# Kernel optimization log

Hardware: AMD Instinct MI355X
Metric: run time of the kernel (lower is better)

Reference implementation:

```python
import jax, jax.numpy as jnp
import numpy as np
import math

DIM = 512
NUM_HEADS = 8
DIM_HEAD = DIM // NUM_HEADS


def normalized_coords(h, w):
    # (h*w, 2) with (x, y) in [0, 1]
    y = jnp.linspace(0.0, 1.0, h)
    x = jnp.linspace(0.0, 1.0, w)
    yg, xg = jnp.meshgrid(y, x, indexing='ij')
    return jnp.stack([xg.ravel(), yg.ravel()], axis=-1)


def rotate_half(x):
    dh = x.shape[-1] // 2
    return jnp.concatenate([-x[..., dh:], x[..., :dh]], axis=-1)


def apply_rope(t, coords):
    # t: (n, heads, seq, dim_head); coords: (seq, 2) (identical across batch)
    dim_half = t.shape[-1] // 2
    freq = 1.0 / (10000.0 ** (jnp.arange(dim_half, dtype=jnp.float32) / dim_half))
    ang_x = coords[:, 0:1] * freq  # (seq, dim_half)
    ang_y = coords[:, 1:2] * freq
    ang = jnp.concatenate([ang_x, ang_y], axis=-1)  # (seq, dim_head)
    cos, sin = jnp.cos(ang), jnp.sin(ang)
    return t * cos + rotate_half(t) * sin


def setup_inputs() -> dict:
    key = jax.random.key(0)
    ks = jax.random.split(key, 12)
    n, Np, d, H, W = 4, 1024, DIM, 64, 64
    s = 0.02
    return {
        'local_feat': jax.random.normal(ks[0], (n, Np, d), jnp.float32),
        'global_feat': jax.random.normal(ks[1], (n, d, H, W), jnp.float32),
        'Wq': jax.random.normal(ks[2], (d, d), jnp.float32) * s,
        'bq': jnp.zeros((d,), jnp.float32),
        'Wk': jax.random.normal(ks[3], (d, d), jnp.float32) * s,
        'bk': jnp.zeros((d,), jnp.float32),
        'Wv': jax.random.normal(ks[4], (d, d), jnp.float32) * s,
        'bv': jnp.zeros((d,), jnp.float32),
        'Wg': jax.random.normal(ks[5], (d, 2 * d), jnp.float32) * s,
        'bg': jnp.zeros((d,), jnp.float32),
        'Wo': jax.random.normal(ks[6], (d, d), jnp.float32) * s,
        'bo': jnp.zeros((d,), jnp.float32),
    }


def reference(local_feat, global_feat, Wq, bq, Wk, bk, Wv, bv, Wg, bg, Wo, bo):
    n, Np, d = local_feat.shape
    _, _, H, W = global_feat.shape
    h, dh = NUM_HEADS, DIM_HEAD
    gf = global_feat.reshape(n, d, H * W).transpose(0, 2, 1)  # (n, HW, d)

    P = int(math.isqrt(Np))
    local_coords = normalized_coords(P, P)      # (Np, 2)
    global_coords = normalized_coords(H, W)     # (HW, 2)

    def proj(x, Wt, b):
        return x @ Wt.T + b

    Q = proj(local_feat, Wq, bq).reshape(n, Np, h, dh).transpose(0, 2, 1, 3)
    K = proj(gf, Wk, bk).reshape(n, H * W, h, dh).transpose(0, 2, 1, 3)
    V = proj(gf, Wv, bv).reshape(n, H * W, h, dh).transpose(0, 2, 1, 3)

    Q = apply_rope(Q, local_coords)
    K = apply_rope(K, global_coords)

    scores = jnp.einsum('bhqd,bhkd->bhqk', Q, K) / math.sqrt(dh)
    attn = jax.nn.softmax(scores, axis=-1)
    ao = jnp.einsum('bhqk,bhkd->bhqd', attn, V)
    ao = ao.transpose(0, 2, 1, 3).reshape(n, Np, d)

    gate = jax.nn.sigmoid(jnp.concatenate([local_feat, ao], axis=-1) @ Wg.T + bg)
    enhanced = local_feat + gate * ao
    return enhanced @ Wo.T + bo
```

## Files before the change

### kernel.cpp

```cpp
#include <hip/hip_runtime.h>
#include <hip/hip_bf16.h>
#include <cstdint>

typedef __hip_bfloat16 BF;
typedef unsigned short ushort_t;
typedef __attribute__((ext_vector_type(8))) __bf16 bf16x8;
typedef __attribute__((ext_vector_type(4))) float f32x4;
typedef __attribute__((ext_vector_type(4))) unsigned uint4v;

__device__ __forceinline__ float bu2f(ushort_t u) {
  return __uint_as_float((unsigned)u << 16);
}
__device__ __forceinline__ unsigned pk2(float a, float b) {
  union { __hip_bfloat162 h; unsigned u; } c;
  c.h = __float22bfloat162_rn(make_float2(a, b));
  return c.u;
}
__device__ __forceinline__ unsigned short f2bu(float f) {
  union { BF b; unsigned short u; } c; c.b = __float2bfloat16(f); return c.u;
}
__device__ __forceinline__ float b2f(BF x) { return __bfloat162float(x); }
__device__ __forceinline__ void rd16f(const float* fp, ushort_t* out) {
#pragma unroll
  for (int j = 0; j < 16; j += 4) {
    float4 v = *(const float4*)(fp + j);
    ((unsigned*)out)[j / 2] = pk2(v.x, v.y);
    ((unsigned*)out)[j / 2 + 1] = pk2(v.z, v.w);
  }
}

#define QS 0.1803368801111f

__global__ __launch_bounds__(256) void prep_k(const float* __restrict__ local,
                                              const float* __restrict__ Wq,
                                              const float* __restrict__ Wk,
                                              const float* __restrict__ Wv,
                                              const float* __restrict__ Wg,
                                              const float* __restrict__ Wo,
                                              BF* __restrict__ localB,
                                              BF* __restrict__ WB) {
  size_t e = ((size_t)blockIdx.x * 256 + threadIdx.x) * 16;
  const float* src;
  BF* dst;
  if (e < 2097152) {
    src = local + e;  dst = localB + e;
  } else {
    size_t f = e - 2097152;
    dst = WB + f;
    if (f < 262144)        src = Wq + f;
    else if (f < 524288)   src = Wk + (f - 262144);
    else if (f < 786432)   src = Wv + (f - 524288);
    else if (f < 1310720)  src = Wg + (f - 786432);
    else                   src = Wo + (f - 1310720);
  }
  ushort_t vals[16];
  rd16f(src, vals);
  *(uint4*)dst = *(uint4*)&vals[0];
  *((uint4*)dst + 1) = *(uint4*)&vals[8];
}

__global__ __launch_bounds__(256) void pre_k(const float* __restrict__ local,
                                             const float* __restrict__ gfeat,
                                             const float* __restrict__ Wq,
                                             const float* __restrict__ bq,
                                             const BF* __restrict__ localB,
                                             const BF* __restrict__ WqB,
                                             BF* __restrict__ gfT,
                                             BF* __restrict__ Qb) {
  __shared__ __align__(16) ushort_t smem[2][64][72];
  const int t = threadIdx.x;
  if (blockIdx.x < 2048) {
    auto T = smem[0];
    const int g = blockIdx.x;
    const int bz = g & 3, mt = (g >> 2) & 63, kt = g >> 8;
    {
      int krow = t >> 2, mg = t & 3;
      ushort_t vals[16];
      rd16f(gfeat + (size_t)bz * 512 * 4096 + (size_t)(kt * 64 + krow) * 4096 +
                mt * 64 + mg * 16,
            vals);
#pragma unroll
      for (int j = 0; j < 16; ++j) T[mg * 16 + j][krow] = vals[j];
    }
    __syncthreads();
    int mrow = t >> 2, kg = t & 3;
    uint4 a = *(const uint4*)&T[mrow][kg * 16];
    uint4 b = *(const uint4*)&T[mrow][kg * 16 + 8];
    size_t o = ((size_t)bz * 4096 + mt * 64 + mrow) * 512 + kt * 64 + kg * 16;
    *(uint4*)&gfT[o] = a;
    *(uint4*)&gfT[o + 8] = b;
    return;
  }
  auto As = smem[0];
  auto Bs = smem[1];
  const int bx = blockIdx.x - 2048;
  const int m0 = (bx & 63) * 64, n0 = (bx >> 6) * 64;
  const int w = t >> 6, lane = t & 63;
  const int quad = lane >> 4, l16 = lane & 15;

  f32x4 acc[4] = {};
  for (int k0 = 0; k0 < 512; k0 += 64) {
    __syncthreads();
    {
      int row = t >> 2, cg = t & 3;
      int kg = k0 + cg * 16;
      if (WqB) {
        const uint4* pa = (const uint4*)(localB + (size_t)(m0 + row) * 512 + kg);
        *(uint4*)&As[row][cg * 16] = pa[0];
        *(uint4*)&As[row][cg * 16 + 8] = pa[1];
        const uint4* pb = (const uint4*)(WqB + (size_t)(n0 + row) * 512 + kg);
        *(uint4*)&Bs[row][cg * 16] = pb[0];
        *(uint4*)&Bs[row][cg * 16 + 8] = pb[1];
      } else {
        ushort_t vals[16];
        rd16f(local + (size_t)(m0 + row) * 512 + kg, vals);
        *(uint4*)&As[row][cg * 16] = *(uint4*)&vals[0];
        *(uint4*)&As[row][cg * 16 + 8] = *(uint4*)&vals[8];
        ushort_t bv[16];
        rd16f(Wq + (size_t)(n0 + row) * 512 + kg, bv);
        *(uint4*)&Bs[row][cg * 16] = *(uint4*)&bv[0];
        *(uint4*)&Bs[row][cg * 16 + 8] = *(uint4*)&bv[8];
      }
    }
    __syncthreads();
#pragma unroll
    for (int kc = 0; kc < 2; ++kc) {
      bf16x8 af = *(const bf16x8*)&As[w * 16 + l16][kc * 32 + quad * 8];
#pragma unroll
      for (int nt = 0; nt < 4; ++nt) {
        bf16x8 bfv = *(const bf16x8*)&Bs[nt * 16 + l16][kc * 32 + quad * 8];
        acc[nt] = __builtin_amdgcn_mfma_f32_16x16x32_bf16(af, bfv, acc[nt], 0, 0, 0);
      }
    }
  }
  const int head = n0 >> 6;
#pragma unroll
  for (int r = 0; r < 4; ++r) {
    int mg = m0 + w * 16 + quad * 4 + r;
    int bb = mg >> 10, qi = mg & 1023;
    float x = (float)(qi & 31) * (1.f / 31.f);
    float y = (float)(qi >> 5) * (1.f / 31.f);
    size_t base = (((size_t)bb * 8 + head) * 1024 + qi) * 64;
#pragma unroll
    for (int j = 0; j < 2; ++j) {
      int c0 = j * 16 + l16;
      float t0 = acc[j][r] + bq[head * 64 + c0];
      float t1 = acc[j + 2][r] + bq[head * 64 + c0 + 32];
      float fr = __expf((float)c0 * (-9.210340371976184f / 32.f));
      float ax = x * fr, ay = y * fr;
      Qb[base + c0] = __float2bfloat16((t0 * __cosf(ax) - t1 * __sinf(ax)) * QS);
      Qb[base + c0 + 32] = __float2bfloat16((t1 * __cosf(ay) + t0 * __sinf(ay)) * QS);
    }
  }
}

__global__ __launch_bounds__(256) void kv_k(const BF* __restrict__ gfT,
                                            const float* __restrict__ Wk,
                                            const float* __restrict__ Wv,
                                            const BF* __restrict__ WkB,
                                            const BF* __restrict__ WvB,
                                            const float* __restrict__ bk,
                                            const float* __restrict__ bv,
                                            BF* __restrict__ Kb,
                                            BF* __restrict__ VTb) {
  __shared__ __align__(16) ushort_t smem[2][128][72];
  auto As = smem[0];
  auto Bs = smem[1];
  const int tid = threadIdx.x;
  const int w = tid >> 6, lane = tid & 63;
  const int quad = lane >> 4, l16 = lane & 15;
  const int wm = w >> 1, wn = w & 1;
  const int g = blockIdx.x;
  const int a = g & 7, y = (g >> 3) & 7, bidx = g >> 6;
  const int m0 = ((bidx << 1) | (a & 1)) * 128;
  const int n0 = y * 128;
  const int bz = a >> 1;

  f32x4 acc[4][4] = {};
  for (int k0 = 0; k0 < 512; k0 += 64) {
    __syncthreads();
#pragma unroll
    for (int u = 0; u < 2; ++u) {
      int unit = tid + u * 256;
      int row = unit >> 2, cg = unit & 3;
      const uint4* p = (const uint4*)(gfT + ((size_t)bz * 4096 + m0 + row) * 512 +
                                      k0 + cg * 16);
      *(uint4*)&As[row][cg * 16] = p[0];
      *(uint4*)&As[row][cg * 16 + 8] = p[1];
    }
    if (WkB) {
      const BF* bb16 = (n0 >= 512) ? WvB : WkB;
      const int nb = (n0 >= 512) ? (n0 - 512) : n0;
#pragma unroll
      for (int u = 0; u < 2; ++u) {
        int unit = tid + u * 256;
        int row = unit >> 2, cg = unit & 3;
        const uint4* p = (const uint4*)(bb16 + (size_t)(nb + row) * 512 +
                                        k0 + cg * 16);
        *(uint4*)&Bs[row][cg * 16] = p[0];
        *(uint4*)&Bs[row][cg * 16 + 8] = p[1];
      }
    } else {
#pragma unroll
      for (int u = 0; u < 2; ++u) {
        int unit = tid + u * 256;
        int row = unit >> 2, cg = unit & 3;
        const float* bsrc = (n0 >= 512) ? Wv : Wk;
        size_t nrow = (n0 >= 512) ? (n0 - 512 + row) : (n0 + row);
        ushort_t vals[16];
        rd16f(bsrc + nrow * 512 + k0 + cg * 16, vals);
        *(uint4*)&Bs[row][cg * 16] = *(uint4*)&vals[0];
        *(uint4*)&Bs[row][cg * 16 + 8] = *(uint4*)&vals[8];
      }
    }
    __syncthreads();
#pragma unroll
    for (int kc = 0; kc < 2; ++kc) {
      bf16x8 af[4], bfv[4];
#pragma unroll
      for (int i = 0; i < 4; ++i) {
        af[i] = *(const bf16x8*)&As[wm * 64 + i * 16 + l16][kc * 32 + quad * 8];
        bfv[i] = *(const bf16x8*)&Bs[wn * 64 + i * 16 + l16][kc * 32 + quad * 8];
      }
#pragma unroll
      for (int mt = 0; mt < 4; ++mt)
#pragma unroll
        for (int nt = 0; nt < 4; ++nt)
          acc[mt][nt] = __builtin_amdgcn_mfma_f32_16x16x32_bf16(af[mt], bfv[nt], acc[mt][nt], 0, 0, 0);
    }
  }
  if (n0 < 512) {
    const int head = (n0 + wn * 64) >> 6;
#pragma unroll
    for (int mt = 0; mt < 4; ++mt)
#pragma unroll
      for (int r = 0; r < 4; ++r) {
        int pg = m0 + wm * 64 + mt * 16 + quad * 4 + r;
        float x = (float)(pg & 63) * (1.f / 63.f);
        float yy = (float)(pg >> 6) * (1.f / 63.f);
        size_t base = (((size_t)bz * 8 + head) * 4096 + pg) * 64;
#pragma unroll
        for (int j = 0; j < 2; ++j) {
          int c0 = j * 16 + l16;
          float t0 = acc[mt][j][r] + bk[head * 64 + c0];
          float t1 = acc[mt][j + 2][r] + bk[head * 64 + c0 + 32];
          float fr = __expf((float)c0 * (-9.210340371976184f / 32.f));
          float ax = x * fr, ay = yy * fr;
          Kb[base + c0] = __float2bfloat16(t0 * __cosf(ax) - t1 * __sinf(ax));
          Kb[base + c0 + 32] = __float2bfloat16(t1 * __cosf(ay) + t0 * __sinf(ay));
        }
      }
  } else {
    const int n0v = n0 - 512;
    __syncthreads();
    ushort_t (*T)[136] = (ushort_t(*)[136]) & smem[0][0][0];
#pragma unroll
    for (int mt = 0; mt < 4; ++mt)
#pragma unroll
      for (int nt = 0; nt < 4; ++nt)
#pragma unroll
        for (int r = 0; r < 4; ++r) {
          int n_l = wn * 64 + nt * 16 + l16;
          int m_l = wm * 64 + mt * 16 + quad * 4 + r;
          T[n_l][m_l] = f2bu(acc[mt][nt][r] + bv[n0v + n_l]);
        }
    __syncthreads();
    int row = tid >> 1, half = tid & 1;
    size_t gbase = (((size_t)bz * 8 + (n0v >> 6) + (row >> 6)) * 64 + (row & 63)) * 4096 +
                   m0 + half * 64;
    uint4* dst = (uint4*)(VTb + gbase);
    const uint4* src = (const uint4*)&T[row][half * 64];
#pragma unroll
    for (int j = 0; j < 8; ++j) dst[j] = src[j];
  }
}

template <int NS>
__global__ __launch_bounds__(256, 4) void attn_k(const BF* __restrict__ Q,
                                                 const BF* __restrict__ K,
                                                 const BF* __restrict__ VT,
                                                 BF* __restrict__ AO,
                                                 BF* __restrict__ Opart,
                                                 float* __restrict__ lpart) {
  __shared__ __align__(16) ushort_t Ks[2][64][64];
  __shared__ __align__(16) ushort_t VTs[3][64][64];

  const int tid = threadIdx.x;
  const int w = tid >> 6, lane = tid & 63;
  const int quad = lane >> 4, l16 = lane & 15;
  const int r3 = l16 & 7;
  const int sc0 = (quad ^ r3) << 3;
  const int sc1 = sc0 ^ 32;

  const int g = blockIdx.x;
  const int bh = g & 31;
  const int qt = (g >> 5) & 7;
  const int ks = g >> 8;
  const int b = bh >> 3, h = bh & 7;
  const int q0 = qt * 128 + w * 32;
  const int kspan = 4096 / NS, kbase = ks * kspan;

  bf16x8 qa[2][2];
#pragma unroll
  for (int qs = 0; qs < 2; ++qs) {
    const BF* qp = Q + (((size_t)bh << 10) + q0 + qs * 16 + l16) * 64 + quad * 8;
    qa[qs][0] = *(const bf16x8*)qp;
    qa[qs][1] = *(const bf16x8*)(qp + 32);
  }
  bf16x8 ones;
#pragma unroll
  for (int j = 0; j < 8; ++j) ones[j] = (__bf16)1.0f;

  const BF* Kp = K + (size_t)bh * 4096 * 64;
  const BF* VTp = VT + (size_t)bh * 64 * 4096;

  f32x4 o[2][4] = {};
  f32x4 ol[2] = {};

  const int srow = tid >> 2, scol = (tid & 3) * 16;
  const int ssc = ((2 * (tid & 3)) ^ (srow & 7)) << 3;
  int vcol[4];
  {
    const int s1 = (tid >> 1) & 1, s0v = tid & 1;
#pragma unroll
    for (int gq = 0; gq < 4; ++gq)
      vcol[gq] = (((s1 * 4 + gq) ^ (srow & 7)) << 3) + s0v * 4;
  }

#define STAGE_V(buf, v0, v1)                                   \
  {                                                            \
    uint2 t_;                                                  \
    t_.x = (v0).x; t_.y = (v0).y; *(uint2*)&VTs[buf][srow][vcol[0]] = t_; \
    t_.x = (v0).z; t_.y = (v0).w; *(uint2*)&VTs[buf][srow][vcol[1]] = t_; \
    t_.x = (v1).x; t_.y = (v1).y; *(uint2*)&VTs[buf][srow][vcol[2]] = t_; \
    t_.x = (v1).z; t_.y = (v1).w; *(uint2*)&VTs[buf][srow][vcol[3]] = t_; \
  }

  {
    const uint4* kp = (const uint4*)(Kp + (size_t)(kbase + srow) * 64 + scol);
    const uint4* vp = (const uint4*)(VTp + (size_t)srow * 4096 + kbase + scol);
    uint4 a = kp[0], bb = kp[1], c = vp[0], d = vp[1];
    *(uint4*)&Ks[0][srow][ssc] = a;  *(uint4*)&Ks[0][srow][ssc ^ 8] = bb;
    STAGE_V(0, c, d);
  }
  __syncthreads();

  bf16x8 pa[2][2];

#define S_PHASE(KRD)                                                          \
  {                                                                           \
    unsigned pu[2][2][4];                                                     \
    _Pragma("unroll") for (int ct = 0; ct < 4; ++ct) {                        \
      const int krow = ct * 16 + l16;                                         \
      bf16x8 kb0 = *(const bf16x8*)&Ks[KRD][krow][sc0];                       \
      bf16x8 kb1 = *(const bf16x8*)&Ks[KRD][krow][sc1];                       \
      _Pragma("unroll") for (int qs = 0; qs < 2; ++qs) {                      \
        f32x4 s = {};                                                         \
        s = __builtin_amdgcn_mfma_f32_16x16x32_bf16(kb0, qa[qs][0], s, 0, 0, 0); \
        s = __builtin_amdgcn_mfma_f32_16x16x32_bf16(kb1, qa[qs][1], s, 0, 0, 0); \
        pu[qs][ct >> 1][(ct & 1) * 2] =                                       \
            pk2(__builtin_exp2f(s[0]), __builtin_exp2f(s[1]));                \
        pu[qs][ct >> 1][(ct & 1) * 2 + 1] =                                   \
            pk2(__builtin_exp2f(s[2]), __builtin_exp2f(s[3]));                \
      }                                                                       \
    }                                                                         \
    _Pragma("unroll") for (int qs = 0; qs < 2; ++qs)                          \
      _Pragma("unroll") for (int kk = 0; kk < 2; ++kk) {                      \
        uint4v u = {pu[qs][kk][0], pu[qs][kk][1], pu[qs][kk][2],              \
                    pu[qs][kk][3]};                                           \
        pa[qs][kk] = __builtin_bit_cast(bf16x8, u);                           \
      }                                                                       \
  }

#define PV_PHASE(VRD)                                                         \
  {                                                                           \
    _Pragma("unroll") for (int qs = 0; qs < 2; ++qs) {                        \
      ol[qs] = __builtin_amdgcn_mfma_f32_16x16x32_bf16(ones, pa[qs][0], ol[qs], 0, 0, 0); \
      ol[qs] = __builtin_amdgcn_mfma_f32_16x16x32_bf16(ones, pa[qs][1], ol[qs], 0, 0, 0); \
    }                                                                         \
    _Pragma("unroll") for (int nt = 0; nt < 4; ++nt) {                        \
      const int vrow = nt * 16 + l16;                                         \
      bf16x8 vb0 = *(const bf16x8*)&VTs[VRD][vrow][sc0];                      \
      bf16x8 vb1 = *(const bf16x8*)&VTs[VRD][vrow][sc1];                      \
      _Pragma("unroll") for (int qs = 0; qs < 2; ++qs) {                      \
        o[qs][nt] = __builtin_amdgcn_mfma_f32_16x16x32_bf16(vb0, pa[qs][0], o[qs][nt], 0, 0, 0); \
        o[qs][nt] = __builtin_amdgcn_mfma_f32_16x16x32_bf16(vb1, pa[qs][1], o[qs][nt], 0, 0, 0); \
      }                                                                       \
    }                                                                         \
  }

  const int nc = kspan / 64;
  {
    uint4 nk0, nk1, nv0, nv1;
    const bool more = (nc > 1);
    if (more) {
      const int c1 = kbase + 64;
      const uint4* kp = (const uint4*)(Kp + (size_t)(c1 + srow) * 64 + scol);
      const uint4* vp = (const uint4*)(VTp + (size_t)srow * 4096 + c1 + scol);
      nk0 = kp[0]; nk1 = kp[1]; nv0 = vp[0]; nv1 = vp[1];
    }
    __builtin_amdgcn_s_setprio(1);
    S_PHASE(0);
    __builtin_amdgcn_s_setprio(0);
    if (more) {
      *(uint4*)&Ks[1][srow][ssc] = nk0;
      *(uint4*)&Ks[1][srow][ssc ^ 8] = nk1;
      STAGE_V(1, nv0, nv1);
    }
    __syncthreads();
  }

  int krd = 1, vrd = 0, vwr = 2;
  for (int c = 1; c < nc; ++c) {
    uint4 nk0, nk1, nv0, nv1;
    const bool more = (c + 1 < nc);
    if (more) {
      const int c1 = kbase + (c + 1) * 64;
      const uint4* kp = (const uint4*)(Kp + (size_t)(c1 + srow) * 64 + scol);
      const uint4* vp = (const uint4*)(VTp + (size_t)srow * 4096 + c1 + scol);
      nk0 = kp[0]; nk1 = kp[1]; nv0 = vp[0]; nv1 = vp[1];
    }
    __builtin_amdgcn_s_setprio(1);
    PV_PHASE(vrd);
    S_PHASE(krd);
    __builtin_amdgcn_s_setprio(0);
    if (more) {
      *(uint4*)&Ks[krd ^ 1][srow][ssc] = nk0;
      *(uint4*)&Ks[krd ^ 1][srow][ssc ^ 8] = nk1;
      STAGE_V(vwr, nv0, nv1);
    }
    __syncthreads();
    krd ^= 1;
    vrd = (vrd == 2) ? 0 : vrd + 1;
    vwr = (vwr == 2) ? 0 : vwr + 1;
  }
  PV_PHASE(vrd);
#undef STAGE_V
#undef S_PHASE
#undef PV_PHASE

#pragma unroll
  for (int qs = 0; qs < 2; ++qs) {
    int qg = q0 + qs * 16 + l16;
    if (NS == 1) {
      float invl = 1.f / ol[qs][0];
#pragma unroll
      for (int nt = 0; nt < 4; ++nt) {
        uint2 uu;
        uu.x = pk2(o[qs][nt][0] * invl, o[qs][nt][1] * invl);
        uu.y = pk2(o[qs][nt][2] * invl, o[qs][nt][3] * invl);
        *(uint2*)(AO + (((size_t)b << 10) + qg) * 512 + h * 64 + nt * 16 + quad * 4) = uu;
      }
    } else {
      if (quad == 0) lpart[ks * 32768 + (bh << 10) + qg] = ol[qs][0];
#pragma unroll
      for (int nt = 0; nt < 4; ++nt) {
        uint2 uu;
        uu.x = pk2(o[qs][nt][0], o[qs][nt][1]);
        uu.y = pk2(o[qs][nt][2], o[qs][nt][3]);
        *(uint2*)(Opart + (size_t)ks * 2097152 + (((size_t)bh << 10) + qg) * 64 +
                  nt * 16 + quad * 4) = uu;
      }
    }
  }
}

template <int NS>
__global__ __launch_bounds__(256) void gate_k(const float* __restrict__ local,
                                              const BF* __restrict__ localB,
                                              const BF* __restrict__ AO,
                                              const BF* __restrict__ Opart,
                                              const float* __restrict__ lpart,
                                              const float* __restrict__ Wg,
                                              const BF* __restrict__ WgB,
                                              const float* __restrict__ bg,
                                              BF* __restrict__ ENH) {
  __shared__ __align__(16) ushort_t As[64][72];
  __shared__ __align__(16) ushort_t Bs[64][72];
  const int tid = threadIdx.x;
  const int w = tid >> 6, lane = tid & 63;
  const int quad = lane >> 4, l16 = lane & 15;
  const int m0 = blockIdx.x * 64, n0 = blockIdx.y * 64;

  f32x4 acc[4] = {};
  float aosv[4][4];
  for (int k0 = 0; k0 < 1024; k0 += 64) {
    __syncthreads();
    {
      int row = tid >> 2, cg = tid & 3;
      int kg = k0 + cg * 16;
      ushort_t vals[16];
      if (kg < 512) {
        if (localB) {
          const uint4* p = (const uint4*)(localB + (size_t)(m0 + row) * 512 + kg);
          *(uint4*)&vals[0] = p[0]; *(uint4*)&vals[8] = p[1];
        } else {
          rd16f(local + (size_t)(m0 + row) * 512 + kg, vals);
        }
      } else {
        int c = kg - 512;
        int hh = c >> 6, dh0 = c & 63;
        int mg = m0 + row;
        size_t bq = (size_t)(((mg >> 10) * 8 + hh) << 10) + (mg & 1023);
        if (NS == 1) {
          const uint4* p = (const uint4*)(AO + (size_t)mg * 512 + c);
          *(uint4*)&vals[0] = p[0]; *(uint4*)&vals[8] = p[1];
        } else {
          float ls = 0.f;
#pragma unroll
          for (int s2 = 0; s2 < NS; ++s2) ls += lpart[s2 * 32768 + bq];
          float inv = 1.f / ls;
          float av[16] = {};
#pragma unroll
          for (int s2 = 0; s2 < NS; ++s2) {
            const ushort_t* op = (const ushort_t*)Opart + (size_t)s2 * 2097152 +
                                 bq * 64 + dh0;
            uint4 u0 = ((const uint4*)op)[0], u1 = ((const uint4*)op)[1];
            const ushort_t* pu = (const ushort_t*)&u0;
#pragma unroll
            for (int j = 0; j < 8; ++j) av[j] += bu2f(pu[j]);
            pu = (const ushort_t*)&u1;
#pragma unroll
            for (int j = 0; j < 8; ++j) av[8 + j] += bu2f(pu[j]);
          }
#pragma unroll
          for (int j = 0; j < 16; j += 2)
            ((unsigned*)vals)[j / 2] = pk2(av[j] * inv, av[j + 1] * inv);
        }
      }
      *(uint4*)&As[row][cg * 16] = *(uint4*)&vals[0];
      *(uint4*)&As[row][cg * 16 + 8] = *(uint4*)&vals[8];
      if (WgB) {
        const uint4* p = (const uint4*)(WgB + (size_t)(n0 + row) * 1024 + kg);
        *(uint4*)&Bs[row][cg * 16] = p[0];
        *(uint4*)&Bs[row][cg * 16 + 8] = p[1];
      } else {
        ushort_t bv[16];
        rd16f(Wg + (size_t)(n0 + row) * 1024 + kg, bv);
        *(uint4*)&Bs[row][cg * 16] = *(uint4*)&bv[0];
        *(uint4*)&Bs[row][cg * 16 + 8] = *(uint4*)&bv[8];
      }
    }
    __syncthreads();
    if (k0 == 512 + n0) {
#pragma unroll
      for (int r = 0; r < 4; ++r)
#pragma unroll
        for (int nt = 0; nt < 4; ++nt)
          aosv[r][nt] = bu2f(As[w * 16 + quad * 4 + r][nt * 16 + l16]);
    }
#pragma unroll
    for (int kc = 0; kc < 2; ++kc) {
      bf16x8 af = *(const bf16x8*)&As[w * 16 + l16][kc * 32 + quad * 8];
#pragma unroll
      for (int nt = 0; nt < 4; ++nt) {
        bf16x8 bfv = *(const bf16x8*)&Bs[nt * 16 + l16][kc * 32 + quad * 8];
        acc[nt] = __builtin_amdgcn_mfma_f32_16x16x32_bf16(af, bfv, acc[nt], 0, 0, 0);
      }
    }
  }
#pragma unroll
  for (int r = 0; r < 4; ++r) {
    int mg = m0 + w * 16 + quad * 4 + r;
#pragma unroll
    for (int nt = 0; nt < 4; ++nt) {
      int ng = n0 + nt * 16 + l16;
      size_t idx = (size_t)mg * 512 + ng;
      float gg = 1.f / (1.f + __expf(-(acc[nt][r] + bg[ng])));
      ENH[idx] = __float2bfloat16(local[idx] + gg * aosv[r][nt]);
    }
  }
}

__global__ __launch_bounds__(256) void out_k(const BF* __restrict__ ENH,
                                             const float* __restrict__ Wo,
                                             const BF* __restrict__ WoB,
                                             const float* __restrict__ bo,
                                             float* __restrict__ out) {
  __shared__ __align__(16) ushort_t As[64][72];
  __shared__ __align__(16) ushort_t Bs[64][72];
  const int tid = threadIdx.x;
  const int w = tid >> 6, lane = tid & 63;
  const int quad = lane >> 4, l16 = lane & 15;
  const int m0 = blockIdx.x * 64, n0 = blockIdx.y * 64;

  f32x4 acc[4] = {};
  for (int k0 = 0; k0 < 512; k0 += 64) {
    __syncthreads();
    {
      int row = tid >> 2, cg = tid & 3;
      int kg = k0 + cg * 16;
      const uint4* p = (const uint4*)(ENH + (size_t)(m0 + row) * 512 + kg);
      *(uint4*)&As[row][cg * 16] = p[0];
      *(uint4*)&As[row][cg * 16 + 8] = p[1];
      if (WoB) {
        const uint4* pb = (const uint4*)(WoB + (size_t)(n0 + row) * 512 + kg);
        *(uint4*)&Bs[row][cg * 16] = pb[0];
        *(uint4*)&Bs[row][cg * 16 + 8] = pb[1];
      } else {
        ushort_t bv[16];
        rd16f(Wo + (size_t)(n0 + row) * 512 + kg, bv);
        *(uint4*)&Bs[row][cg * 16] = *(uint4*)&bv[0];
        *(uint4*)&Bs[row][cg * 16 + 8] = *(uint4*)&bv[8];
      }
    }
    __syncthreads();
#pragma unroll
    for (int kc = 0; kc < 2; ++kc) {
      bf16x8 af = *(const bf16x8*)&As[w * 16 + l16][kc * 32 + quad * 8];
#pragma unroll
      for (int nt = 0; nt < 4; ++nt) {
        bf16x8 bfv = *(const bf16x8*)&Bs[nt * 16 + l16][kc * 32 + quad * 8];
        acc[nt] = __builtin_amdgcn_mfma_f32_16x16x32_bf16(af, bfv, acc[nt], 0, 0, 0);
      }
    }
  }
#pragma unroll
  for (int r = 0; r < 4; ++r) {
    int mg = m0 + w * 16 + quad * 4 + r;
#pragma unroll
    for (int nt = 0; nt < 4; ++nt) {
      int ng = n0 + nt * 16 + l16;
      out[(size_t)mg * 512 + ng] = acc[nt][r] + bo[ng];
    }
  }
}

extern "C" void kernel_launch(void* const* d_in, const int* in_sizes, int n_in,
                              void* d_out, int out_size, void* d_ws, size_t ws_size,
                              hipStream_t stream) {
  const float* local = (const float*)d_in[0];
  const float* gfeat = (const float*)d_in[1];
  const float* Wq = (const float*)d_in[2];
  const float* bq = (const float*)d_in[3];
  const float* Wk = (const float*)d_in[4];
  const float* bk = (const float*)d_in[5];
  const float* Wv = (const float*)d_in[6];
  const float* bv = (const float*)d_in[7];
  const float* Wg = (const float*)d_in[8];
  const float* bg = (const float*)d_in[9];
  const float* Wo = (const float*)d_in[10];
  const float* bo = (const float*)d_in[11];

  char* w = (char*)d_ws;
  BF* Qb = (BF*)w;            w += (size_t)2097152 * 2;
  BF* Kb = (BF*)w;            w += (size_t)8388608 * 2;
  BF* VTb = (BF*)w;           w += (size_t)8388608 * 2;
  BF* AO = (BF*)w;            w += (size_t)2097152 * 2;
  BF* gfT = (BF*)w;
  BF* Opart = (BF*)w;
  size_t baseOff = (size_t)(w - (char*)d_ws);
  BF* ENH = Qb;

  int NS = 1;
  if (baseOff + 4 * (4194304 + 131072) <= ws_size) NS = 4;
  else if (baseOff + 16777216 + 2 * 131072 <= ws_size) NS = 2;
  float* lpart = (float*)(w + (size_t)NS * 4194304);

  size_t xsize = (size_t)NS * (4194304 + 131072);
  if (xsize < 16777216) xsize = 16777216;
  BF* WB = (BF*)(w + xsize);
  BF* localB = WB + 1572864;
  bool useP = (baseOff + xsize + 3145728 + 4194304) <= ws_size;
  const BF *WqB = nullptr, *WkB = nullptr, *WvB = nullptr, *WgB = nullptr,
           *WoB = nullptr, *locB = nullptr;
  if (useP) {
    WqB = WB;            WkB = WB + 262144;  WvB = WB + 524288;
    WgB = WB + 786432;   WoB = WB + 1310720; locB = localB;
  }

  dim3 blk(256);
  if (useP)
    prep_k<<<dim3(896), blk, 0, stream>>>(local, Wq, Wk, Wv, Wg, Wo, localB, WB);
  pre_k<<<dim3(2560), blk, 0, stream>>>(local, gfeat, Wq, bq, locB, WqB, gfT, Qb);
  kv_k<<<dim3(1024), blk, 0, stream>>>(gfT, Wk, Wv, WkB, WvB, bk, bv, Kb, VTb);
  if (NS == 4) {
    attn_k<4><<<dim3(1024), blk, 0, stream>>>(Qb, Kb, VTb, AO, Opart, lpart);
    gate_k<4><<<dim3(64, 8), blk, 0, stream>>>(local, locB, AO, Opart, lpart, Wg, WgB, bg, ENH);
  } else if (NS == 2) {
    attn_k<2><<<dim3(512), blk, 0, stream>>>(Qb, Kb, VTb, AO, Opart, lpart);
    gate_k<2><<<dim3(64, 8), blk, 0, stream>>>(local, locB, AO, Opart, lpart, Wg, WgB, bg, ENH);
  } else {
    attn_k<1><<<dim3(256), blk, 0, stream>>>(Qb, Kb, VTb, AO, nullptr, nullptr);
    gate_k<1><<<dim3(64, 8), blk, 0, stream>>>(local, locB, AO, Opart, lpart, Wg, WgB, bg, ENH);
  }
  out_k<<<dim3(64, 8), blk, 0, stream>>>(ENH, Wo, WoB, bo, (float*)d_out);
}
```

Before: 239.1 us.

## Use 512-thread attention blocks sharing K/V tiles and add 8-way key split

The attention kernel now runs 8 waves per block, each handling 32 queries, so one staged 64-key K/V tile in LDS serves 256 queries instead of 128. This halves per-query global and LDS staging traffic, and each thread loads one 16-byte chunk per tile instead of two. A new NS=8 key-split path is chosen when workspace allows, keeping the grid at 1024 blocks, and AO now aliases the scratch region. The cost is more partial outputs for the gate kernel to merge, plus more register pressure from the tighter launch bounds.

Result: slower. 405.9 us (+69.7%).

```diff
diff --git a/kernel.cpp b/kernel.cpp
--- a/kernel.cpp
+++ b/kernel.cpp
@@ -276,7 +276,7 @@
 }
 
 template <int NS>
-__global__ __launch_bounds__(256, 4) void attn_k(const BF* __restrict__ Q,
+__global__ __launch_bounds__(512, 8) void attn_k(const BF* __restrict__ Q,
                                                  const BF* __restrict__ K,
                                                  const BF* __restrict__ VT,
                                                  BF* __restrict__ AO,
@@ -294,10 +294,10 @@
 
   const int g = blockIdx.x;
   const int bh = g & 31;
-  const int qt = (g >> 5) & 7;
-  const int ks = g >> 8;
+  const int qt = (g >> 5) & 3;
+  const int ks = g >> 7;
   const int b = bh >> 3, h = bh & 7;
-  const int q0 = qt * 128 + w * 32;
+  const int q0 = qt * 256 + w * 32;
   const int kspan = 4096 / NS, kbase = ks * kspan;
 
   bf16x8 qa[2][2];
@@ -317,31 +317,28 @@
   f32x4 o[2][4] = {};
   f32x4 ol[2] = {};
 
-  const int srow = tid >> 2, scol = (tid & 3) * 16;
-  const int ssc = ((2 * (tid & 3)) ^ (srow & 7)) << 3;
-  int vcol[4];
+  const int srow = tid >> 3, scol = (tid & 7) * 8;
+  const int ssc = ((tid & 7) ^ (srow & 7)) << 3;
+  int vcol[2];
   {
-    const int s1 = (tid >> 1) & 1, s0v = tid & 1;
-#pragma unroll
-    for (int gq = 0; gq < 4; ++gq)
-      vcol[gq] = (((s1 * 4 + gq) ^ (srow & 7)) << 3) + s0v * 4;
-  }
-
-#define STAGE_V(buf, v0, v1)                                   \
+    const int s2 = (tid >> 2) & 1, s1 = (tid >> 1) & 1, s0v = tid & 1;
+#pragma unroll
+    for (int j2 = 0; j2 < 2; ++j2)
+      vcol[j2] = (((s2 * 4 + s0v * 2 + j2) ^ (srow & 7)) << 3) + s1 * 4;
+  }
+
+#define STAGE_V(buf, v0)                                       \
   {                                                            \
     uint2 t_;                                                  \
     t_.x = (v0).x; t_.y = (v0).y; *(uint2*)&VTs[buf][srow][vcol[0]] = t_; \
     t_.x = (v0).z; t_.y = (v0).w; *(uint2*)&VTs[buf][srow][vcol[1]] = t_; \
-    t_.x = (v1).x; t_.y = (v1).y; *(uint2*)&VTs[buf][srow][vcol[2]] = t_; \
-    t_.x = (v1).z; t_.y = (v1).w; *(uint2*)&VTs[buf][srow][vcol[3]] = t_; \
   }
 
   {
-    const uint4* kp = (const uint4*)(Kp + (size_t)(kbase + srow) * 64 + scol);
-    const uint4* vp = (const uint4*)(VTp + (size_t)srow * 4096 + kbase + scol);
-    uint4 a = kp[0], bb = kp[1], c = vp[0], d = vp[1];
-    *(uint4*)&Ks[0][srow][ssc] = a;  *(uint4*)&Ks[0][srow][ssc ^ 8] = bb;
-    STAGE_V(0, c, d);
+    uint4 a = *(const uint4*)(Kp + (size_t)(kbase + srow) * 64 + scol);
+    uint4 c = *(const uint4*)(VTp + (size_t)srow * 4096 + kbase + scol);
+    *(uint4*)&Ks[0][srow][ssc] = a;
+    STAGE_V(0, c);
   }
   __syncthreads();
 
@@ -391,34 +388,31 @@
 
   const int nc = kspan / 64;
   {
-    uint4 nk0, nk1, nv0, nv1;
+    uint4 nk0, nv0;
     const bool more = (nc > 1);
     if (more) {
       const int c1 = kbase + 64;
-      const uint4* kp = (const uint4*)(Kp + (size_t)(c1 + srow) * 64 + scol);
-      const uint4* vp = (const uint4*)(VTp + (size_t)srow * 4096 + c1 + scol);
-      nk0 = kp[0]; nk1 = kp[1]; nv0 = vp[0]; nv1 = vp[1];
+      nk0 = *(const uint4*)(Kp + (size_t)(c1 + srow) * 64 + scol);
+      nv0 = *(const uint4*)(VTp + (size_t)srow * 4096 + c1 + scol);
     }
     __builtin_amdgcn_s_setprio(1);
     S_PHASE(0);
     __builtin_amdgcn_s_setprio(0);
     if (more) {
       *(uint4*)&Ks[1][srow][ssc] = nk0;
-      *(uint4*)&Ks[1][srow][ssc ^ 8] = nk1;
-      STAGE_V(1, nv0, nv1);
+      STAGE_V(1, nv0);
     }
     __syncthreads();
   }
 
   int krd = 1, vrd = 0, vwr = 2;
   for (int c = 1; c < nc; ++c) {
-    uint4 nk0, nk1, nv0, nv1;
+    uint4 nk0, nv0;
     const bool more = (c + 1 < nc);
     if (more) {
       const int c1 = kbase + (c + 1) * 64;
-      const uint4* kp = (const uint4*)(Kp + (size_t)(c1 + srow) * 64 + scol);
-      const uint4* vp = (const uint4*)(VTp + (size_t)srow * 4096 + c1 + scol);
-      nk0 = kp[0]; nk1 = kp[1]; nv0 = vp[0]; nv1 = vp[1];
+      nk0 = *(const uint4*)(Kp + (size_t)(c1 + srow) * 64 + scol);
+      nv0 = *(const uint4*)(VTp + (size_t)srow * 4096 + c1 + scol);
     }
     __builtin_amdgcn_s_setprio(1);
     PV_PHASE(vrd);
@@ -426,8 +420,7 @@
     __builtin_amdgcn_s_setprio(0);
     if (more) {
       *(uint4*)&Ks[krd ^ 1][srow][ssc] = nk0;
-      *(uint4*)&Ks[krd ^ 1][srow][ssc ^ 8] = nk1;
-      STAGE_V(vwr, nv0, nv1);
+      STAGE_V(vwr, nv0);
     }
     __syncthreads();
     krd ^= 1;
@@ -646,22 +639,25 @@
   BF* Qb = (BF*)w;            w += (size_t)2097152 * 2;
   BF* Kb = (BF*)w;            w += (size_t)8388608 * 2;
   BF* VTb = (BF*)w;           w += (size_t)8388608 * 2;
-  BF* AO = (BF*)w;            w += (size_t)2097152 * 2;
   BF* gfT = (BF*)w;
   BF* Opart = (BF*)w;
+  BF* AO = (BF*)w;
   size_t baseOff = (size_t)(w - (char*)d_ws);
   BF* ENH = Qb;
 
+  const size_t perNS = 4194304 + 131072;
+  const size_t prepSz = 3145728 + 4194304;
   int NS = 1;
-  if (baseOff + 4 * (4194304 + 131072) <= ws_size) NS = 4;
+  if (baseOff + 8 * perNS + prepSz <= ws_size) NS = 8;
+  else if (baseOff + 4 * perNS + prepSz <= ws_size) NS = 4;
   else if (baseOff + 16777216 + 2 * 131072 <= ws_size) NS = 2;
   float* lpart = (float*)(w + (size_t)NS * 4194304);
 
-  size_t xsize = (size_t)NS * (4194304 + 131072);
+  size_t xsize = (size_t)NS * perNS;
   if (xsize < 16777216) xsize = 16777216;
   BF* WB = (BF*)(w + xsize);
   BF* localB = WB + 1572864;
-  bool useP = (baseOff + xsize + 3145728 + 4194304) <= ws_size;
+  bool useP = (baseOff + xsize + prepSz) <= ws_size;
   const BF *WqB = nullptr, *WkB = nullptr, *WvB = nullptr, *WgB = nullptr,
            *WoB = nullptr, *locB = nullptr;
   if (useP) {
@@ -670,18 +666,22 @@
   }
 
   dim3 blk(256);
+  dim3 ablk(512);
   if (useP)
     prep_k<<<dim3(896), blk, 0, stream>>>(local, Wq, Wk, Wv, Wg, Wo, localB, WB);
   pre_k<<<dim3(2560), blk, 0, stream>>>(local, gfeat, Wq, bq, locB, WqB, gfT, Qb);
   kv_k<<<dim3(1024), blk, 0, stream>>>(gfT, Wk, Wv, WkB, WvB, bk, bv, Kb, VTb);
-  if (NS == 4) {
-    attn_k<4><<<dim3(1024), blk, 0, stream>>>(Qb, Kb, VTb, AO, Opart, lpart);
+  if (NS == 8) {
+    attn_k<8><<<dim3(1024), ablk, 0, stream>>>(Qb, Kb, VTb, AO, Opart, lpart);
+    gate_k<8><<<dim3(64, 8), blk, 0, stream>>>(local, locB, AO, Opart, lpart, Wg, WgB, bg, ENH);
+  } else if (NS == 4) {
+    attn_k<4><<<dim3(512), ablk, 0, stream>>>(Qb, Kb, VTb, AO, Opart, lpart);
     gate_k<4><<<dim3(64, 8), blk, 0, stream>>>(local, locB, AO, Opart, lpart, Wg, WgB, bg, ENH);
   } else if (NS == 2) {
-    attn_k<2><<<dim3(512), blk, 0, stream>>>(Qb, Kb, VTb, AO, Opart, lpart);
+    attn_k<2><<<dim3(256), ablk, 0, stream>>>(Qb, Kb, VTb, AO, Opart, lpart);
     gate_k<2><<<dim3(64, 8), blk, 0, stream>>>(local, locB, AO, Opart, lpart, Wg, WgB, bg, ENH);
   } else {
-    attn_k<1><<<dim3(256), blk, 0, stream>>>(Qb, Kb, VTb, AO, nullptr, nullptr);
+    attn_k<1><<<dim3(128), ablk, 0, stream>>>(Qb, Kb, VTb, AO, nullptr, nullptr);
     gate_k<1><<<dim3(64, 8), blk, 0, stream>>>(local, locB, AO, Opart, lpart, Wg, WgB, bg, ENH);
   }
   out_k<<<dim3(64, 8), blk, 0, stream>>>(ENH, Wo, WoB, bo, (float*)d_out);
```
